# Optimization experiments

Measured on AMD Instinct MI355X. Metric: run time of the kernel, lower is better.

The kernel has to match this reference:

```python
import jax, jax.numpy as jnp
import numpy as np

K = 20          # neighbors, default of knn/get_graph_feature
EPS = 1e-5      # BatchNorm eps (torch default)


def knn_idx(x, k):
    # x: [B,3,N] -> indices of k nearest neighbors [B,N,k]
    xx = jnp.sum(x * x, axis=1)                      # [B,N]
    inner = jnp.einsum('bdn,bdm->bnm', x, x)         # [B,N,N]
    neg_dist = 2.0 * inner - xx[:, :, None] - xx[:, None, :]  # -||xi-xj||^2
    return jax.lax.top_k(neg_dist, k)[1]             # largest == nearest


def graph_feature(x, k):
    # x: [B,D,N] -> [B,2D,N,k]  (channels = [neighbor feats, center feats])
    idx = knn_idx(x, k)                              # [B,N,k]
    xt = jnp.transpose(x, (0, 2, 1))                 # [B,N,D]
    nbr = jax.vmap(lambda p, i: p[i])(xt, idx)       # [B,N,k,D] gather
    ctr = jnp.broadcast_to(xt[:, :, None, :], nbr.shape)
    feat = jnp.concatenate([nbr, ctr], axis=3)       # [B,N,k,2D]
    return jnp.transpose(feat, (0, 3, 1, 2))         # [B,2D,N,k]


def conv1x1(y, W):
    # Conv2d(kernel_size=1, bias=False): y [B,C,N,k], W [O,C]
    return jnp.einsum('bcnk,oc->bonk', y, W)


def bn_relu(y, g, b):
    # BatchNorm2d in training mode (batch statistics over B,N,k per channel)
    m = jnp.mean(y, axis=(0, 2, 3), keepdims=True)
    v = jnp.mean((y - m) ** 2, axis=(0, 2, 3), keepdims=True)
    yn = (y - m) * jax.lax.rsqrt(v + EPS)
    return jax.nn.relu(yn * g[None, :, None, None] + b[None, :, None, None])


def setup_inputs() -> dict:
    key = jax.random.key(0)
    ks = jax.random.split(key, 20)
    B, D, N = 8, 3, 2048
    x = jax.random.normal(ks[0], (B, D, N), dtype=jnp.float32)
    def w(k, o, c):
        return jax.random.normal(k, (o, c), dtype=jnp.float32) * (1.0 / np.sqrt(c))
    inp = {
        'x': x,
        'W1': w(ks[1], 64, 6),   'W2': w(ks[2], 64, 64),
        'W3': w(ks[3], 128, 64), 'W4': w(ks[4], 256, 128),
        'W5': w(ks[5], 512, 512),
    }
    for i, c in zip(range(1, 6), (64, 64, 128, 256, 512)):
        inp[f'g{i}'] = 1.0 + 0.1 * jax.random.normal(ks[5 + i], (c,), dtype=jnp.float32)
        inp[f'b{i}'] = 0.1 * jax.random.normal(ks[10 + i], (c,), dtype=jnp.float32)
    return inp


def reference(x, W1, W2, W3, W4, W5, g1, b1, g2, b2, g3, b3, g4, b4, g5, b5):
    # DGCNN core: single kNN graph feature + 4 EdgeConv 1x1 convs with
    # per-layer max over neighbors, concat, final 1x1 conv, pad to 1024 ch.
    f = graph_feature(x, K)                          # [B,6,N,K]
    h1 = bn_relu(conv1x1(f, W1), g1, b1)             # [B,64,N,K]
    x1 = jnp.max(h1, axis=-1, keepdims=True)
    h2 = bn_relu(conv1x1(h1, W2), g2, b2)            # [B,64,N,K]
    x2 = jnp.max(h2, axis=-1, keepdims=True)
    h3 = bn_relu(conv1x1(h2, W3), g3, b3)            # [B,128,N,K]
    x3 = jnp.max(h3, axis=-1, keepdims=True)
    h4 = bn_relu(conv1x1(h3, W4), g4, b4)            # [B,256,N,K]
    x4 = jnp.max(h4, axis=-1, keepdims=True)
    cat = jnp.concatenate([x1, x2, x3, x4], axis=1)  # [B,512,N,1]
    h5 = bn_relu(conv1x1(cat, W5), g5, b5)[..., 0]   # [B,512,N]
    out = jnp.pad(h5, ((0, 0), (0, 1024 - 512), (0, 0)))  # pad channels -> 1024
    return out.astype(jnp.float32)
```

## Files before the change

kernel.cpp:

```cpp
#include <hip/hip_runtime.h>

#define BB  8
#define NP  2048
#define KNB 20
#define KP  10
#define SS  40960

typedef unsigned short bf16_t;
typedef __attribute__((ext_vector_type(8))) short short8_t;
typedef __attribute__((ext_vector_type(4))) float f32x4;

static __device__ __forceinline__ float bf2f(unsigned short u) {
    return __uint_as_float(((unsigned)u) << 16);
}
static __device__ __forceinline__ bf16_t f2bf(float f) {
    unsigned u = __float_as_uint(f);
    return (bf16_t)((u + 0x7fffu + ((u >> 16) & 1u)) >> 16);
}

#if __has_builtin(__builtin_amdgcn_fmed3f)
#define MED3(a, b, c) __builtin_amdgcn_fmed3f((a), (b), (c))
#else
#define MED3(a, b, c) fmaxf(fminf((a), (b)), fminf(fmaxf((a), (b)), (c)))
#endif

static __device__ __forceinline__ float negdist(float4 me, float4 p) {
    float d = me.x * p.x + me.y * p.y + me.z * p.z;
    return 2.0f * d - me.w - p.w;
}

#define BDECL(t) float bv##t = -3.4e38f;
#define MCH(t, p) bv##t = MED3(v, bv##p, bv##t);
#define BSHIFT(t, n) bv##t = bv##n;
#define FDECL(t) float fv##t = -3.4e38f;
#define FMCH(t, p) fv##t = MED3(v, fv##p, fv##t);
#define FSHIFT(t, n) fv##t = fv##n;

__global__ __launch_bounds__(256) void knn_kernel(const float* __restrict__ x,
                                                  int* __restrict__ idx) {
    __shared__ float4 tile[2064];
    __shared__ int   cnt[16];
    __shared__ float svv[16][44];
    __shared__ int   svj[16][44];
    const int tid  = threadIdx.x;
    const int b    = blockIdx.x >> 7;
    const int pblk = blockIdx.x & 127;
    const int pl   = tid >> 4;
    const int seg  = tid & 15;
    const int i    = pblk * 16 + pl;
    const float* xb = x + (size_t)b * 3 * NP;

    for (int j = tid; j < NP; j += 256) {
        float a0 = xb[j], a1 = xb[NP + j], a2 = xb[2 * NP + j];
        tile[j + (j >> 7)] = make_float4(a0, a1, a2, a0 * a0 + a1 * a1 + a2 * a2);
    }
    if (tid < 16) cnt[tid] = 0;
    __syncthreads();
    const float4 me = tile[i + (i >> 7)];
    const float4* tseg = &tile[seg * 129];

    BDECL(0) BDECL(1) BDECL(2) BDECL(3) BDECL(4)
    BDECL(5) BDECL(6) BDECL(7) BDECL(8) BDECL(9)
    for (int t = 0; t < 128; ++t) {
        float v = negdist(me, tseg[t]);
        MCH(9,8) MCH(8,7) MCH(7,6) MCH(6,5) MCH(5,4)
        MCH(4,3) MCH(3,2) MCH(2,1) MCH(1,0)
        bv0 = fmaxf(bv0, v);
    }

    float theta = -3.4e38f;
    int pops = 0;
    for (int r = 0; r < KNB; ++r) {
        float mv = bv0; int ms = seg;
#pragma unroll
        for (int s = 1; s <= 8; s <<= 1) {
            float ov = __shfl_xor(mv, s, 64);
            int   os = __shfl_xor(ms, s, 64);
            if (ov > mv || (ov == mv && os < ms)) { mv = ov; ms = os; }
        }
        if (seg == ms) {
            BSHIFT(0,1) BSHIFT(1,2) BSHIFT(2,3) BSHIFT(3,4) BSHIFT(4,5)
            BSHIFT(5,6) BSHIFT(6,7) BSHIFT(7,8) BSHIFT(8,9)
            bv9 = -3.4e38f;
            ++pops;
        }
        theta = mv;
    }

    int bad = (pops >= KP) ? 1 : 0;
#pragma unroll
    for (int s = 1; s <= 8; s <<= 1) bad |= __shfl_xor(bad, s, 64);
    if (bad) {
        FDECL(0)  FDECL(1)  FDECL(2)  FDECL(3)  FDECL(4)
        FDECL(5)  FDECL(6)  FDECL(7)  FDECL(8)  FDECL(9)
        FDECL(10) FDECL(11) FDECL(12) FDECL(13) FDECL(14)
        FDECL(15) FDECL(16) FDECL(17) FDECL(18) FDECL(19)
        for (int t = 0; t < 128; ++t) {
            float v = negdist(me, tseg[t]);
            FMCH(19,18) FMCH(18,17) FMCH(17,16) FMCH(16,15) FMCH(15,14)
            FMCH(14,13) FMCH(13,12) FMCH(12,11) FMCH(11,10) FMCH(10,9)
            FMCH(9,8)   FMCH(8,7)   FMCH(7,6)   FMCH(6,5)   FMCH(5,4)
            FMCH(4,3)   FMCH(3,2)   FMCH(2,1)   FMCH(1,0)
            fv0 = fmaxf(fv0, v);
        }
        theta = -3.4e38f;
        for (int r = 0; r < KNB; ++r) {
            float mv = fv0; int ms = seg;
#pragma unroll
            for (int s = 1; s <= 8; s <<= 1) {
                float ov = __shfl_xor(mv, s, 64);
                int   os = __shfl_xor(ms, s, 64);
                if (ov > mv || (ov == mv && os < ms)) { mv = ov; ms = os; }
            }
            if (seg == ms) {
                FSHIFT(0,1)   FSHIFT(1,2)   FSHIFT(2,3)   FSHIFT(3,4)   FSHIFT(4,5)
                FSHIFT(5,6)   FSHIFT(6,7)   FSHIFT(7,8)   FSHIFT(8,9)   FSHIFT(9,10)
                FSHIFT(10,11) FSHIFT(11,12) FSHIFT(12,13) FSHIFT(13,14) FSHIFT(14,15)
                FSHIFT(15,16) FSHIFT(16,17) FSHIFT(17,18) FSHIFT(18,19)
                fv19 = -3.4e38f;
            }
            theta = mv;
        }
    }

    for (int t = 0; t < 128; ++t) {
        float v = negdist(me, tseg[t]);
        if (v >= theta) {
            int k = atomicAdd(&cnt[pl], 1);
            if (k < 44) { svv[pl][k] = v; svj[pl][k] = seg * 128 + t; }
        }
    }
    __syncthreads();

    int n = cnt[pl]; if (n > 44) n = 44;
    int* o = idx + ((size_t)b * NP + i) * KNB;
    for (int e = seg; e < n; e += 16) {
        float v = svv[pl][e]; int j = svj[pl][e];
        int rank = 0;
        for (int q = 0; q < n; ++q) {
            float vq = svv[pl][q]; int jq = svj[pl][q];
            rank += (vq > v || (vq == v && jq < j)) ? 1 : 0;
        }
        if (rank < KNB) o[rank] = j;
    }
}

__global__ void gather_kernel(const float* __restrict__ x, const int* __restrict__ idx,
                              bf16_t* __restrict__ f) {
    int s = blockIdx.x * 256 + threadIdx.x;
    int b = blockIdx.y;
    int n = s / KNB;
    int j = idx[(size_t)b * SS + s];
    const float* xb = x + (size_t)b * 3 * NP;
    ushort4 u0, u1;
    u0.x = f2bf(xb[j]);          u0.y = f2bf(xb[NP + j]);
    u0.z = f2bf(xb[2 * NP + j]); u0.w = f2bf(xb[n]);
    u1.x = f2bf(xb[NP + n]);     u1.y = f2bf(xb[2 * NP + n]);
    u1.z = 0; u1.w = 0;
    ushort4 z4; z4.x = 0; z4.y = 0; z4.z = 0; z4.w = 0;
    bf16_t* fb = f + ((size_t)b * SS + s) * 32;
    *(ushort4*)(fb)      = u0;
    *(ushort4*)(fb + 4)  = u1;
    *(ushort4*)(fb + 8)  = z4;
    *(ushort4*)(fb + 12) = z4;
    *(ushort4*)(fb + 16) = z4;
    *(ushort4*)(fb + 20) = z4;
    *(ushort4*)(fb + 24) = z4;
    *(ushort4*)(fb + 28) = z4;
}

__global__ void wconv_kernel(const float* __restrict__ src, bf16_t* __restrict__ dst,
                             int O, int CI, int CIP) {
    int t = blockIdx.x * 256 + threadIdx.x;
    if (t >= O * CIP) return;
    int o = t / CIP, cp = t - o * CIP;
    dst[t] = (cp < CI) ? f2bf(src[o * CI + cp]) : (bf16_t)0;
}

__global__ void zstats_kernel(float* __restrict__ p) {
    p[blockIdx.x * 256 + threadIdx.x] = 0.f;
}

__global__ void bnrelu_kernel(bf16_t* __restrict__ y, const float* __restrict__ ab,
                              int C) {
    size_t e0 = ((size_t)blockIdx.x * 256 + threadIdx.x) * 8;
    int c0 = (int)(e0 & (size_t)(C - 1));
    uint4 r = *(uint4*)(y + e0);
    float4 a0 = *(const float4*)(ab + c0);
    float4 a1 = *(const float4*)(ab + c0 + 4);
    float4 d0 = *(const float4*)(ab + C + c0);
    float4 d1 = *(const float4*)(ab + C + c0 + 4);
    float v0 = bf2f((unsigned short)(r.x & 0xffffu)), v1 = bf2f((unsigned short)(r.x >> 16));
    float v2 = bf2f((unsigned short)(r.y & 0xffffu)), v3 = bf2f((unsigned short)(r.y >> 16));
    float v4 = bf2f((unsigned short)(r.z & 0xffffu)), v5 = bf2f((unsigned short)(r.z >> 16));
    float v6 = bf2f((unsigned short)(r.w & 0xffffu)), v7 = bf2f((unsigned short)(r.w >> 16));
    v0 = fmaxf(fmaf(a0.x, v0, d0.x), 0.f); v1 = fmaxf(fmaf(a0.y, v1, d0.y), 0.f);
    v2 = fmaxf(fmaf(a0.z, v2, d0.z), 0.f); v3 = fmaxf(fmaf(a0.w, v3, d0.w), 0.f);
    v4 = fmaxf(fmaf(a1.x, v4, d1.x), 0.f); v5 = fmaxf(fmaf(a1.y, v5, d1.y), 0.f);
    v6 = fmaxf(fmaf(a1.z, v6, d1.z), 0.f); v7 = fmaxf(fmaf(a1.w, v7, d1.w), 0.f);
    r.x = (unsigned)f2bf(v0) | ((unsigned)f2bf(v1) << 16);
    r.y = (unsigned)f2bf(v2) | ((unsigned)f2bf(v3) << 16);
    r.z = (unsigned)f2bf(v4) | ((unsigned)f2bf(v5) << 16);
    r.w = (unsigned)f2bf(v6) | ((unsigned)f2bf(v7) << 16);
    *(uint4*)(y + e0) = r;
}

#define MF(A, B, C) C = __builtin_amdgcn_mfma_f32_16x16x32_bf16(A, B, C, 0, 0, 0);

#define LGKM_BARRIER() { \
    asm volatile("s_waitcnt lgkmcnt(0)" ::: "memory"); \
    __builtin_amdgcn_s_barrier(); \
    asm volatile("" ::: "memory"); }

#define TILE1(CC, CT, STt, YT) { \
    ushort4 t4; \
    t4.x = f2bf(CC[0]); t4.y = f2bf(CC[1]); \
    t4.z = f2bf(CC[2]); t4.w = f2bf(CC[3]); \
    *(ushort4*)&YT[w * 32 + (STt) * 16 + col][(CT) * 16 + quad * 4] = t4; }

#define EPILOGUE(ITV) { \
    bf16_t (*yt)[68] = ytile[(ITV) & (NBUF - 1)]; \
    TILE1(c00,0,0,yt) TILE1(c10,1,0,yt) TILE1(c20,2,0,yt) TILE1(c30,3,0,yt) \
    TILE1(c01,0,1,yt) TILE1(c11,1,1,yt) TILE1(c21,2,1,yt) TILE1(c31,3,1,yt) \
    LGKM_BARRIER() \
    if constexpr (ST) { \
        const int row0 = blockIdx.x * (SR * NS) + (ITV) * SR; \
        for (int i = tid; i < SR * 16; i += NW * 64) { \
            int row = i >> 4, c4 = (i & 15) * 4; \
            ushort4 yv = *(const ushort4*)&yt[row][c4]; \
            *(ushort4*)(Yout + ((size_t)b * SROWS + row0 + row) * COUT_T + cob + c4) = yv; \
            if constexpr (!POOL) { \
                float v0 = bf2f(yv.x), v1 = bf2f(yv.y); \
                float v2 = bf2f(yv.z), v3 = bf2f(yv.w); \
                sv0 += v0; qv0 = fmaf(v0, v0, qv0); \
                sv1 += v1; qv1 = fmaf(v1, v1, qv1); \
                sv2 += v2; qv2 = fmaf(v2, v2, qv2); \
                sv3 += v3; qv3 = fmaf(v3, v3, qv3); \
            } \
        } \
    } \
    if constexpr (POOL) { \
        const int nbase = (blockIdx.x * NS + (ITV)) * 8; \
        for (int i = tid; i < 8 * 32; i += NW * 64) { \
            const int nl = i >> 5, c2 = (i & 31) * 2; \
            float m0 = -3.4e38f, m1 = -3.4e38f; \
            _Pragma("unroll") \
            for (int k = 0; k < KNB; ++k) { \
                unsigned u = *(const unsigned*)&yt[nl * 20 + k][c2]; \
                float v0 = bf2f((unsigned short)(u & 0xffffu)); \
                float v1 = bf2f((unsigned short)(u >> 16)); \
                m0 = fmaxf(m0, v0); m1 = fmaxf(m1, v1); \
                svA += v0; qvA = fmaf(v0, v0, qvA); \
                svB += v1; qvB = fmaf(v1, v1, qvB); \
            } \
            unsigned r2 = (unsigned)f2bf(m0) | ((unsigned)f2bf(m1) << 16); \
            *(unsigned*)(poolOut + ((size_t)b * NP + nbase + nl) * 512 + chofs + cob + c2) = r2; \
        } \
    } \
}

template<int CIN, int COUT_T, int SROWS, int NW, int NS, bool POOL, bool ST, bool PRE>
__global__ __launch_bounds__(320)
void mconv(const bf16_t* __restrict__ H, const bf16_t* __restrict__ Wb,
           bf16_t* __restrict__ Yout, bf16_t* __restrict__ poolOut,
           int chofs, float* __restrict__ stats) {
    constexpr int SR = NW * 32;
    constexpr int NKK = CIN / 32;
    constexpr int NBUF = (NS > 1) ? 2 : 1;
    __shared__ bf16_t ytile[NBUF][SR][68];
    __shared__ float redS[NW][64];
    __shared__ float redQ[NW][64];
    const int tid  = threadIdx.x;
    const int lane = tid & 63, col = lane & 15, quad = lane >> 4, q8 = quad * 8;
    const int w    = tid >> 6;
    const int cob  = blockIdx.y * 64;
    const int b    = blockIdx.z;
    const bf16_t* wp = Wb + (size_t)(cob + col) * CIN + q8;

    float svA = 0.f, svB = 0.f, qvA = 0.f, qvB = 0.f;
    float sv0 = 0.f, sv1 = 0.f, sv2 = 0.f, sv3 = 0.f;
    float qv0 = 0.f, qv1 = 0.f, qv2 = 0.f, qv3 = 0.f;

    if constexpr (PRE) {
        short8_t Af0[NKK], Af1[NKK], Af2[NKK], Af3[NKK];
#pragma unroll
        for (int kk = 0; kk < NKK; ++kk) {
            Af0[kk] = *(const short8_t*)(wp + kk * 32);
            Af1[kk] = *(const short8_t*)(wp + 16 * CIN + kk * 32);
            Af2[kk] = *(const short8_t*)(wp + 32 * CIN + kk * 32);
            Af3[kk] = *(const short8_t*)(wp + 48 * CIN + kk * 32);
        }

        short8_t cb0[NKK], cb1[NKK], nb0[NKK], nb1[NKK];
        {
            const int sb = blockIdx.x * (SR * NS) + w * 32;
            const bf16_t* hp0 = H + ((size_t)b * SROWS + sb + col) * CIN + q8;
            const bf16_t* hp1 = hp0 + 16 * CIN;
#pragma unroll
            for (int kk = 0; kk < NKK; ++kk) {
                cb0[kk] = *(const short8_t*)(hp0 + kk * 32);
                cb1[kk] = *(const short8_t*)(hp1 + kk * 32);
            }
        }

#pragma unroll 1
        for (int it = 0; it < NS; ++it) {
            if (it + 1 < NS) {
                const int sb = blockIdx.x * (SR * NS) + (it + 1) * SR + w * 32;
                const bf16_t* hp0 = H + ((size_t)b * SROWS + sb + col) * CIN + q8;
                const bf16_t* hp1 = hp0 + 16 * CIN;
#pragma unroll
                for (int kk = 0; kk < NKK; ++kk) {
                    nb0[kk] = *(const short8_t*)(hp0 + kk * 32);
                    nb1[kk] = *(const short8_t*)(hp1 + kk * 32);
                }
            }

            f32x4 c00 = {0.f,0.f,0.f,0.f}, c10 = c00, c20 = c00, c30 = c00;
            f32x4 c01 = c00, c11 = c00, c21 = c00, c31 = c00;
#pragma unroll
            for (int kk = 0; kk < NKK; ++kk) {
                MF(Af0[kk], cb0[kk], c00) MF(Af1[kk], cb0[kk], c10)
                MF(Af2[kk], cb0[kk], c20) MF(Af3[kk], cb0[kk], c30)
                MF(Af0[kk], cb1[kk], c01) MF(Af1[kk], cb1[kk], c11)
                MF(Af2[kk], cb1[kk], c21) MF(Af3[kk], cb1[kk], c31)
            }

            EPILOGUE(it)

            if (it + 1 < NS) {
#pragma unroll
                for (int kk = 0; kk < NKK; ++kk) { cb0[kk] = nb0[kk]; cb1[kk] = nb1[kk]; }
            }
        }
    } else {
        for (int it = 0; it < NS; ++it) {
            const int sb = blockIdx.x * (SR * NS) + it * SR + w * 32;
            const bf16_t* hp0 = H + ((size_t)b * SROWS + sb + col) * CIN + q8;
            const bf16_t* hp1 = hp0 + 16 * CIN;

            f32x4 c00 = {0.f,0.f,0.f,0.f}, c10 = c00, c20 = c00, c30 = c00;
            f32x4 c01 = c00, c11 = c00, c21 = c00, c31 = c00;

            short8_t a0c = *(const short8_t*)(wp);
            short8_t a1c = *(const short8_t*)(wp + 16 * CIN);
            short8_t a2c = *(const short8_t*)(wp + 32 * CIN);
            short8_t a3c = *(const short8_t*)(wp + 48 * CIN);
            short8_t b0c = *(const short8_t*)(hp0);
            short8_t b1c = *(const short8_t*)(hp1);

#pragma unroll 1
            for (int k0 = 0; k0 < CIN; k0 += 32) {
                short8_t a0n, a1n, a2n, a3n, b0n, b1n;
                if (k0 + 32 < CIN) {
                    a0n = *(const short8_t*)(wp + k0 + 32);
                    a1n = *(const short8_t*)(wp + 16 * CIN + k0 + 32);
                    a2n = *(const short8_t*)(wp + 32 * CIN + k0 + 32);
                    a3n = *(const short8_t*)(wp + 48 * CIN + k0 + 32);
                    b0n = *(const short8_t*)(hp0 + k0 + 32);
                    b1n = *(const short8_t*)(hp1 + k0 + 32);
                }
                MF(a0c, b0c, c00) MF(a1c, b0c, c10) MF(a2c, b0c, c20) MF(a3c, b0c, c30)
                MF(a0c, b1c, c01) MF(a1c, b1c, c11) MF(a2c, b1c, c21) MF(a3c, b1c, c31)
                if (k0 + 32 < CIN) {
                    a0c = a0n; a1c = a1n; a2c = a2n; a3c = a3n;
                    b0c = b0n; b1c = b1n;
                }
            }

            EPILOGUE(it)
        }
    }

    if constexpr (POOL) {
        svA += __shfl_xor(svA, 32, 64); qvA += __shfl_xor(qvA, 32, 64);
        svB += __shfl_xor(svB, 32, 64); qvB += __shfl_xor(qvB, 32, 64);
        if (lane < 32) {
            const int c2 = lane * 2;
            redS[w][c2] = svA; redS[w][c2 + 1] = svB;
            redQ[w][c2] = qvA; redQ[w][c2 + 1] = qvB;
        }
    } else if constexpr (ST) {
        sv0 += __shfl_xor(sv0, 16, 64); qv0 += __shfl_xor(qv0, 16, 64);
        sv1 += __shfl_xor(sv1, 16, 64); qv1 += __shfl_xor(qv1, 16, 64);
        sv2 += __shfl_xor(sv2, 16, 64); qv2 += __shfl_xor(qv2, 16, 64);
        sv3 += __shfl_xor(sv3, 16, 64); qv3 += __shfl_xor(qv3, 16, 64);
        sv0 += __shfl_xor(sv0, 32, 64); qv0 += __shfl_xor(qv0, 32, 64);
        sv1 += __shfl_xor(sv1, 32, 64); qv1 += __shfl_xor(qv1, 32, 64);
        sv2 += __shfl_xor(sv2, 32, 64); qv2 += __shfl_xor(qv2, 32, 64);
        sv3 += __shfl_xor(sv3, 32, 64); qv3 += __shfl_xor(qv3, 32, 64);
        if (lane < 16) {
            const int c4 = lane * 4;
            redS[w][c4]     = sv0; redS[w][c4 + 1] = sv1;
            redS[w][c4 + 2] = sv2; redS[w][c4 + 3] = sv3;
            redQ[w][c4]     = qv0; redQ[w][c4 + 1] = qv1;
            redQ[w][c4 + 2] = qv2; redQ[w][c4 + 3] = qv3;
        }
    }
    __syncthreads();
    if (tid < 64) {
        float sv = 0.f, qv = 0.f;
#pragma unroll
        for (int ch = 0; ch < NW; ++ch) { sv += redS[ch][tid]; qv += redQ[ch][tid]; }
        atomicAdd(&stats[cob + tid], sv);
        atomicAdd(&stats[COUT_T + cob + tid], qv);
    }
}

__global__ void bn_finalize(const float* __restrict__ stats,
                            const float* __restrict__ g, const float* __restrict__ bt,
                            float* __restrict__ ab, int C, float invM) {
    int c = blockIdx.x * 64 + threadIdx.x;
    if (c >= C) return;
    float mean = stats[c] * invM;
    float var  = fmaxf(stats[C + c] * invM - mean * mean, 0.f);
    float a = g[c] * rsqrtf(var + 1e-5f);
    ab[c] = a;
    ab[C + c] = fmaf(-mean, a, bt[c]);
}

__global__ void pool_convert(const bf16_t* __restrict__ pr, const float* __restrict__ ab,
                             bf16_t* __restrict__ xc, int C, int chofs, int logC) {
    int t = blockIdx.x * 256 + threadIdx.x;
    int c = t & (C - 1);
    int rest = t >> logC;
    int n = rest & (NP - 1);
    int b = rest >> 11;
    size_t p = ((size_t)b * NP + n) * 512 + chofs + c;
    float v = bf2f(pr[p]);
    xc[p] = f2bf(fmaxf(fmaf(ab[c], v, ab[C + c]), 0.f));
}

__global__ void out_kernel(const bf16_t* __restrict__ y5, const float* __restrict__ ab,
                           float* __restrict__ out) {
    int t = blockIdx.x * 256 + threadIdx.x;
    int n = t & (NP - 1);
    int c4 = (t >> 11) & 255;
    int b = t >> 19;
    int c0 = c4 * 4;
    float4 v = make_float4(0.f, 0.f, 0.f, 0.f);
    if (c0 < 512) {
        ushort4 yv = *(const ushort4*)(y5 + ((size_t)b * NP + n) * 512 + c0);
        float4 av = *(const float4*)(ab + c0);
        float4 dv = *(const float4*)(ab + 512 + c0);
        v.x = fmaxf(fmaf(av.x, bf2f(yv.x), dv.x), 0.f);
        v.y = fmaxf(fmaf(av.y, bf2f(yv.y), dv.y), 0.f);
        v.z = fmaxf(fmaf(av.z, bf2f(yv.z), dv.z), 0.f);
        v.w = fmaxf(fmaf(av.w, bf2f(yv.w), dv.w), 0.f);
    }
    float* ob = out + ((size_t)b * 1024 + c0) * NP + n;
    ob[0] = v.x; ob[NP] = v.y; ob[2 * NP] = v.z; ob[3 * NP] = v.w;
}

extern "C" void kernel_launch(void* const* d_in, const int* in_sizes, int n_in,
                              void* d_out, int out_size, void* d_ws, size_t ws_size,
                              hipStream_t stream) {
    (void)in_sizes; (void)n_in; (void)out_size; (void)ws_size;
    const float* x  = (const float*)d_in[0];
    const float* W1 = (const float*)d_in[1];
    const float* W2 = (const float*)d_in[2];
    const float* W3 = (const float*)d_in[3];
    const float* W4 = (const float*)d_in[4];
    const float* W5 = (const float*)d_in[5];
    const float* g1 = (const float*)d_in[6];  const float* b1 = (const float*)d_in[7];
    const float* g2 = (const float*)d_in[8];  const float* b2 = (const float*)d_in[9];
    const float* g3 = (const float*)d_in[10]; const float* b3 = (const float*)d_in[11];
    const float* g4 = (const float*)d_in[12]; const float* b4 = (const float*)d_in[13];
    const float* g5 = (const float*)d_in[14]; const float* b5 = (const float*)d_in[15];

    char* ws = (char*)d_ws;
    bf16_t* f    = (bf16_t*)(ws + 0);
    bf16_t* y2   = (bf16_t*)(ws + 0);
    bf16_t* y5   = (bf16_t*)(ws + 0);
    bf16_t* y1   = (bf16_t*)(ws + 41943040);
    bf16_t* y3   = (bf16_t*)(ws + 41943040);
    bf16_t* poolraw = (bf16_t*)(ws + 125829120);
    bf16_t* xcat    = (bf16_t*)(ws + 142606336);
    bf16_t* Wball   = (bf16_t*)(ws + 159383552);
    bf16_t* W1b = Wball;
    bf16_t* W2b = Wball + 2048;
    bf16_t* W3b = Wball + 6144;
    bf16_t* W4b = Wball + 14336;
    bf16_t* W5b = Wball + 47104;
    float* stats = (float*)(ws + 160002048);
    float* ab    = (float*)(ws + 160010240);
    int*  idx    = (int*)  (ws + 160018432);

    float* st1 = stats;        float* st2 = stats + 128;  float* st3 = stats + 256;
    float* st4 = stats + 512;  float* st5 = stats + 1024;
    float* ab1 = ab;       float* ab2 = ab + 128;  float* ab3 = ab + 256;
    float* ab4 = ab + 512; float* ab5 = ab + 1024;
    const float invM14 = 1.f / (float)(BB * SS);
    const float invM5  = 1.f / (float)(BB * NP);

    zstats_kernel<<<8, 256, 0, stream>>>(stats);
    wconv_kernel<<<8,    256, 0, stream>>>(W1, W1b, 64, 6, 32);
    wconv_kernel<<<16,   256, 0, stream>>>(W2, W2b, 64, 64, 64);
    wconv_kernel<<<32,   256, 0, stream>>>(W3, W3b, 128, 64, 64);
    wconv_kernel<<<128,  256, 0, stream>>>(W4, W4b, 256, 128, 128);
    wconv_kernel<<<1024, 256, 0, stream>>>(W5, W5b, 512, 512, 512);

    knn_kernel<<<1024, 256, 0, stream>>>(x, idx);
    gather_kernel<<<dim3(160, BB), 256, 0, stream>>>(x, idx, f);

    mconv<32, 64, SS, 5, 8, true, true, true><<<dim3(32, 1, BB), 320, 0, stream>>>(
        f, W1b, y1, poolraw, 0, st1);
    bn_finalize<<<1, 64, 0, stream>>>(st1, g1, b1, ab1, 64, invM14);
    pool_convert<<<4096, 256, 0, stream>>>(poolraw, ab1, xcat, 64, 0, 6);
    bnrelu_kernel<<<10240, 256, 0, stream>>>(y1, ab1, 64);

    mconv<64, 64, SS, 5, 8, true, true, true><<<dim3(32, 1, BB), 320, 0, stream>>>(
        y1, W2b, y2, poolraw, 64, st2);
    bn_finalize<<<1, 64, 0, stream>>>(st2, g2, b2, ab2, 64, invM14);
    pool_convert<<<4096, 256, 0, stream>>>(poolraw, ab2, xcat, 64, 64, 6);
    bnrelu_kernel<<<10240, 256, 0, stream>>>(y2, ab2, 64);

    mconv<64, 128, SS, 5, 8, true, true, true><<<dim3(32, 2, BB), 320, 0, stream>>>(
        y2, W3b, y3, poolraw, 128, st3);
    bn_finalize<<<2, 64, 0, stream>>>(st3, g3, b3, ab3, 128, invM14);
    pool_convert<<<8192, 256, 0, stream>>>(poolraw, ab3, xcat, 128, 128, 7);
    bnrelu_kernel<<<20480, 256, 0, stream>>>(y3, ab3, 128);

    mconv<128, 256, SS, 5, 16, true, false, true><<<dim3(16, 4, BB), 320, 0, stream>>>(
        y3, W4b, nullptr, poolraw, 256, st4);
    bn_finalize<<<4, 64, 0, stream>>>(st4, g4, b4, ab4, 256, invM14);
    pool_convert<<<16384, 256, 0, stream>>>(poolraw, ab4, xcat, 256, 256, 8);

    mconv<512, 512, NP, 4, 1, false, true, false><<<dim3(16, 8, BB), 256, 0, stream>>>(
        xcat, W5b, y5, nullptr, 0, st5);
    bn_finalize<<<8, 64, 0, stream>>>(st5, g5, b5, ab5, 512, invM5);

    out_kernel<<<16384, 256, 0, stream>>>(y5, ab5, (float*)d_out);
}
```

Baseline: 423.8 us.

## Shrink kNN partial buffer, transpose output through LDS, split zero padding

The per-segment kNN candidate buffer drops from 10 to 7 entries. This cuts compare-insert work in the main scan, but the exact fallback path will be taken more often when one segment holds many neighbors. The output kernel now stages a 32-point by 512-channel tile in shared memory so that both reading the bf16 y5 and writing the transposed fp32 output are coalesced and vectorized. The zero padding for channels 512 to 1023 moves into a separate early kernel, so the final kernel only writes the live half.

```diff
diff --git a/kernel.cpp b/kernel.cpp
--- a/kernel.cpp
+++ b/kernel.cpp
@@ -3,7 +3,7 @@
 #define BB  8
 #define NP  2048
 #define KNB 20
-#define KP  10
+#define KP  7
 #define SS  40960
 
 typedef unsigned short bf16_t;
@@ -59,12 +59,10 @@
     const float4 me = tile[i + (i >> 7)];
     const float4* tseg = &tile[seg * 129];
 
-    BDECL(0) BDECL(1) BDECL(2) BDECL(3) BDECL(4)
-    BDECL(5) BDECL(6) BDECL(7) BDECL(8) BDECL(9)
+    BDECL(0) BDECL(1) BDECL(2) BDECL(3) BDECL(4) BDECL(5) BDECL(6)
     for (int t = 0; t < 128; ++t) {
         float v = negdist(me, tseg[t]);
-        MCH(9,8) MCH(8,7) MCH(7,6) MCH(6,5) MCH(5,4)
-        MCH(4,3) MCH(3,2) MCH(2,1) MCH(1,0)
+        MCH(6,5) MCH(5,4) MCH(4,3) MCH(3,2) MCH(2,1) MCH(1,0)
         bv0 = fmaxf(bv0, v);
     }
 
@@ -79,9 +77,8 @@
             if (ov > mv || (ov == mv && os < ms)) { mv = ov; ms = os; }
         }
         if (seg == ms) {
-            BSHIFT(0,1) BSHIFT(1,2) BSHIFT(2,3) BSHIFT(3,4) BSHIFT(4,5)
-            BSHIFT(5,6) BSHIFT(6,7) BSHIFT(7,8) BSHIFT(8,9)
-            bv9 = -3.4e38f;
+            BSHIFT(0,1) BSHIFT(1,2) BSHIFT(2,3) BSHIFT(3,4) BSHIFT(4,5) BSHIFT(5,6)
+            bv6 = -3.4e38f;
             ++pops;
         }
         theta = mv;
@@ -431,25 +428,57 @@
     xc[p] = f2bf(fmaxf(fmaf(ab[c], v, ab[C + c]), 0.f));
 }
 
-__global__ void out_kernel(const bf16_t* __restrict__ y5, const float* __restrict__ ab,
-                           float* __restrict__ out) {
-    int t = blockIdx.x * 256 + threadIdx.x;
-    int n = t & (NP - 1);
-    int c4 = (t >> 11) & 255;
-    int b = t >> 19;
-    int c0 = c4 * 4;
-    float4 v = make_float4(0.f, 0.f, 0.f, 0.f);
-    if (c0 < 512) {
-        ushort4 yv = *(const ushort4*)(y5 + ((size_t)b * NP + n) * 512 + c0);
-        float4 av = *(const float4*)(ab + c0);
-        float4 dv = *(const float4*)(ab + 512 + c0);
-        v.x = fmaxf(fmaf(av.x, bf2f(yv.x), dv.x), 0.f);
-        v.y = fmaxf(fmaf(av.y, bf2f(yv.y), dv.y), 0.f);
-        v.z = fmaxf(fmaf(av.z, bf2f(yv.z), dv.z), 0.f);
-        v.w = fmaxf(fmaf(av.w, bf2f(yv.w), dv.w), 0.f);
-    }
-    float* ob = out + ((size_t)b * 1024 + c0) * NP + n;
-    ob[0] = v.x; ob[NP] = v.y; ob[2 * NP] = v.z; ob[3 * NP] = v.w;
+__global__ __launch_bounds__(256) void out_kernel(const bf16_t* __restrict__ y5,
+                                                  const float* __restrict__ ab,
+                                                  float* __restrict__ out) {
+    __shared__ float lds[32][512];
+    const int t  = threadIdx.x;
+    const int nb = blockIdx.x * 32;
+    const int b  = blockIdx.y;
+#pragma unroll
+    for (int k = 0; k < 8; ++k) {
+        int ch  = t + k * 256;
+        int row = ch >> 6;
+        int c8  = (ch & 63) * 8;
+        const bf16_t* yp = y5 + ((size_t)b * NP + nb + row) * 512 + c8;
+        ushort4 u0 = *(const ushort4*)(yp);
+        ushort4 u1 = *(const ushort4*)(yp + 4);
+        float4 a0 = *(const float4*)(ab + c8);
+        float4 a1 = *(const float4*)(ab + c8 + 4);
+        float4 d0 = *(const float4*)(ab + 512 + c8);
+        float4 d1 = *(const float4*)(ab + 512 + c8 + 4);
+        lds[row][c8 + 0] = fmaxf(fmaf(a0.x, bf2f(u0.x), d0.x), 0.f);
+        lds[row][c8 + 1] = fmaxf(fmaf(a0.y, bf2f(u0.y), d0.y), 0.f);
+        lds[row][c8 + 2] = fmaxf(fmaf(a0.z, bf2f(u0.z), d0.z), 0.f);
+        lds[row][c8 + 3] = fmaxf(fmaf(a0.w, bf2f(u0.w), d0.w), 0.f);
+        lds[row][c8 + 4] = fmaxf(fmaf(a1.x, bf2f(u1.x), d1.x), 0.f);
+        lds[row][c8 + 5] = fmaxf(fmaf(a1.y, bf2f(u1.y), d1.y), 0.f);
+        lds[row][c8 + 6] = fmaxf(fmaf(a1.z, bf2f(u1.z), d1.z), 0.f);
+        lds[row][c8 + 7] = fmaxf(fmaf(a1.w, bf2f(u1.w), d1.w), 0.f);
+    }
+    __syncthreads();
+    const int n4   = t & 7;
+    const int crow = t >> 3;
+#pragma unroll
+    for (int cc = 0; cc < 16; ++cc) {
+        int c = crow + cc * 32;
+        float4 v;
+        v.x = lds[n4 * 4 + 0][c];
+        v.y = lds[n4 * 4 + 1][c];
+        v.z = lds[n4 * 4 + 2][c];
+        v.w = lds[n4 * 4 + 3][c];
+        *(float4*)(out + ((size_t)b * 1024 + c) * NP + nb + n4 * 4) = v;
+    }
+}
+
+__global__ void zout_kernel(float* __restrict__ out) {
+    size_t idx4 = (size_t)blockIdx.x * 256 + threadIdx.x;
+    size_t off  = idx4 * 4;
+    size_t per_b = (size_t)512 * NP;
+    size_t b = off / per_b;
+    size_t r = off - b * per_b;
+    float4 z = make_float4(0.f, 0.f, 0.f, 0.f);
+    *(float4*)(out + (b * 1024 + 512) * NP + r) = z;
 }
 
 extern "C" void kernel_launch(void* const* d_in, const int* in_sizes, int n_in,
@@ -503,6 +532,8 @@
     knn_kernel<<<1024, 256, 0, stream>>>(x, idx);
     gather_kernel<<<dim3(160, BB), 256, 0, stream>>>(x, idx, f);
 
+    zout_kernel<<<8192, 256, 0, stream>>>((float*)d_out);
+
     mconv<32, 64, SS, 5, 8, true, true, true><<<dim3(32, 1, BB), 320, 0, stream>>>(
         f, W1b, y1, poolraw, 0, st1);
     bn_finalize<<<1, 64, 0, stream>>>(st1, g1, b1, ab1, 64, invM14);
@@ -530,5 +561,5 @@
         xcat, W5b, y5, nullptr, 0, st5);
     bn_finalize<<<8, 64, 0, stream>>>(st5, g5, b5, ab5, 512, invM5);
 
-    out_kernel<<<16384, 256, 0, stream>>>(y5, ab5, (float*)d_out);
-}
+    out_kernel<<<dim3(64, BB), 256, 0, stream>>>(y5, ab5, (float*)d_out);
+}
```

Result: slower. 439.0 us (+3.6%).
